# Optimization experiments

Hardware: AMD Instinct MI355X
Metric: run time of the kernel (lower is better)

Reference implementation:

```python
import jax, jax.numpy as jnp
import numpy as np

DIM, NH, WS, SS = 192, 6, 8, 4
B, H, W = 4, 192, 192
MID = max(DIM // 16, 4)
N = WS * WS
HD = DIM // NH
SCALE = HD ** -0.5

def _rel_index():
    coords = np.stack(np.meshgrid(np.arange(WS), np.arange(WS), indexing='ij')).reshape(2, -1)
    rel = (coords[:, :, None] - coords[:, None, :]).transpose(1, 2, 0)
    rel[..., 0] += WS - 1
    rel[..., 1] += WS - 1
    rel[..., 0] *= 2 * WS - 1
    return rel.sum(-1)  # (N, N)

REL_IDX = jnp.asarray(_rel_index())

def _shift_mask():
    img = np.zeros((1, H, W, 1), np.float32)
    sl = (slice(0, -WS), slice(-WS, -SS), slice(-SS, None))
    cnt = 0
    for hs in sl:
        for ws_ in sl:
            img[:, hs, ws_, :] = cnt
            cnt += 1
    mw = img.reshape(1, H // WS, WS, W // WS, WS, 1).transpose(0, 1, 3, 2, 4, 5).reshape(-1, N)
    am = mw[:, None, :] - mw[:, :, None]
    return jnp.asarray(np.where(am != 0, -100.0, 0.0).astype(np.float32))  # (nW, N, N)

MASK = _shift_mask()

def _win_part(x):  # (B,H,W,C) -> (B*nW, N, C)
    Bb, Hh, Ww, C = x.shape
    x = x.reshape(Bb, Hh // WS, WS, Ww // WS, WS, C).transpose(0, 1, 3, 2, 4, 5)
    return x.reshape(-1, N, C)

def _win_rev(x, Bb):  # (B*nW, N, C) -> (B,H,W,C)
    x = x.reshape(Bb, H // WS, W // WS, WS, WS, -1).transpose(0, 1, 3, 2, 4, 5)
    return x.reshape(Bb, H, W, -1)

def _ln(x, g, b):
    mu = x.mean(-1, keepdims=True)
    var = ((x - mu) ** 2).mean(-1, keepdims=True)
    return (x - mu) * jax.lax.rsqrt(var + 1e-5) * g + b

def _conv(x, w, b, groups=1):
    y = jax.lax.conv_general_dilated(x, w, (1, 1), 'SAME',
        dimension_numbers=('NCHW', 'OIHW', 'NCHW'), feature_group_count=groups)
    return y + b[None, :, None, None]

def _gelu(x):
    return jax.nn.gelu(x, approximate=False)  # torch default GELU is exact erf


def setup_inputs() -> dict:
    key = jax.random.key(0)
    ks = jax.random.split(key, 12)
    s = 0.02
    return {
        'x': jax.random.normal(ks[0], (B, DIM, H, W), jnp.float32),
        'norm1_g': jnp.ones((DIM,), jnp.float32),
        'norm1_b': jnp.zeros((DIM,), jnp.float32),
        'qkv_w': jax.random.normal(ks[1], (3 * DIM, DIM), jnp.float32) * s,
        'qkv_b': jnp.zeros((3 * DIM,), jnp.float32),
        'rel_table': jax.random.normal(ks[2], ((2 * WS - 1) ** 2, NH), jnp.float32) * s,
        'norm2_g': jnp.ones((DIM,), jnp.float32),
        'norm2_b': jnp.zeros((DIM,), jnp.float32),
        'mlp_w1': jax.random.normal(ks[3], (4 * DIM, DIM), jnp.float32) * s,
        'mlp_b1': jnp.zeros((4 * DIM,), jnp.float32),
        'mlp_w2': jax.random.normal(ks[4], (DIM, 4 * DIM), jnp.float32) * s,
        'mlp_b2': jnp.zeros((DIM,), jnp.float32),
        'ca_c1_w': jax.random.normal(ks[5], (DIM, DIM, 3, 3), jnp.float32) * s,
        'ca_c1_b': jnp.zeros((DIM,), jnp.float32),
        'ca_c2_w': jax.random.normal(ks[6], (DIM, DIM, 3, 3), jnp.float32) * s,
        'ca_c2_b': jnp.zeros((DIM,), jnp.float32),
        'se_w1': jax.random.normal(ks[7], (MID, DIM), jnp.float32) * s,
        'se_b1': jnp.zeros((MID,), jnp.float32),
        'se_w2': jax.random.normal(ks[8], (DIM, MID), jnp.float32) * s,
        'se_b2': jnp.zeros((DIM,), jnp.float32),
        'gate_w': jax.random.normal(ks[9], (DIM, 1, 3, 3), jnp.float32) * s,
        'gate_b': jnp.zeros((DIM,), jnp.float32),
    }


def reference(x, norm1_g, norm1_b, qkv_w, qkv_b, rel_table, norm2_g, norm2_b,
              mlp_w1, mlp_b1, mlp_w2, mlp_b2, ca_c1_w, ca_c1_b, ca_c2_w, ca_c2_b,
              se_w1, se_b1, se_w2, se_b2, gate_w, gate_b):
    Bb = x.shape[0]
    shortcut = x
    xh = _ln(x.transpose(0, 2, 3, 1), norm1_g, norm1_b)  # (B,H,W,C)
    xh = jnp.roll(xh, (-SS, -SS), (1, 2))                # shifted windows
    xw = _win_part(xh)                                   # (B*nW, N, C)
    qkv = jnp.einsum('bnc,dc->bnd', xw, qkv_w) + qkv_b
    qkv = qkv.reshape(-1, N, 3, NH, HD).transpose(2, 0, 3, 1, 4)
    q, k, v = qkv[0], qkv[1], qkv[2]                     # (B_, NH, N, HD)
    attn = jnp.einsum('bhnd,bhmd->bhnm', q * SCALE, k)
    bias = rel_table[REL_IDX.reshape(-1)].reshape(N, N, NH).transpose(2, 0, 1)
    attn = attn + bias[None]
    nW = MASK.shape[0]
    attn = attn.reshape(Bb, nW, NH, N, N) + MASK[None, :, None]
    attn = jax.nn.softmax(attn.reshape(-1, NH, N, N), axis=-1)
    out = jnp.einsum('bhnm,bhmd->bhnd', attn, v).transpose(0, 2, 1, 3).reshape(-1, N, DIM)
    # NOTE: original forward never applies self.proj; faithfully omitted.
    xh = _win_rev(out, Bb)
    xh = jnp.roll(xh, (SS, SS), (1, 2))
    x = shortcut + xh.transpose(0, 3, 1, 2)
    x = x + _conv(x, gate_w, gate_b, groups=DIM)         # depthwise conv gate
    # channel attention (conv body + SE)
    res = x
    y = _conv(x, ca_c1_w, ca_c1_b)
    y = _gelu(y)
    y = _conv(y, ca_c2_w, ca_c2_b)
    p = y.mean((2, 3))                                   # global avg pool -> (B,C)
    wgt = jax.nn.sigmoid(jax.nn.relu(p @ se_w1.T + se_b1) @ se_w2.T + se_b2)
    x = y * wgt[:, :, None, None] + res
    # MLP
    res = x
    xh = _ln(x.transpose(0, 2, 3, 1), norm2_g, norm2_b)
    xh = _gelu(jnp.einsum('bhwc,dc->bhwd', xh, mlp_w1) + mlp_b1)
    xh = jnp.einsum('bhwd,cd->bhwc', xh, mlp_w2) + mlp_b2
    return res + xh.transpose(0, 3, 1, 2)
```

## Files before the change

kernel.cpp:

```cpp
#include <hip/hip_runtime.h>
#include <hip/hip_bf16.h>

#define NWIN 576
#define SP 36864
#define ATT_SCALE 0.17677669529663687f

typedef unsigned short u16;
typedef unsigned int u32;
typedef __attribute__((ext_vector_type(8))) __bf16 bf16x8;
typedef __attribute__((ext_vector_type(4))) float f32x4;

__device__ __forceinline__ float b2f(u16 u){ return __uint_as_float(((u32)u)<<16); }
__device__ __forceinline__ u16 f2b(float f){ u32 u = __float_as_uint(f); return (u16)((u + 0x7FFFu + ((u>>16)&1u)) >> 16); }
__device__ __forceinline__ float fast_rcp(float d){ float r; asm("v_rcp_f32 %0, %1" : "=v"(r) : "v"(d)); return r; }
__device__ __forceinline__ u32 cvtpk(float lo, float hi){ u32 r; asm("v_cvt_pk_bf16_f32 %0, %1, %2" : "=v"(r) : "v"(lo), "v"(hi)); return r; }
__device__ __forceinline__ float gelu_f(float v){
  float u = v*(1.5957691216f + 0.0713548163f*v*v);
  return v * fast_rcp(1.0f + __expf(-u));
}
__device__ __forceinline__ f32x4 mfma16(bf16x8 a, bf16x8 b, f32x4 c){
  return __builtin_amdgcn_mfma_f32_16x16x32_bf16(a, b, c, 0, 0, 0);
}

__global__ __launch_bounds__(256) void k_transpose(const float* __restrict__ x, u16* __restrict__ xn){
  __shared__ float tile[32][33];
  int blk = blockIdx.x;
  int b = blk / 1728; int rem = blk % 1728;
  int hg = rem / 36; int rem2 = rem % 36;
  int wt = rem2 / 6, ct = rem2 % 6;
  int t = threadIdx.x;
  int lw = t & 31, g = t >> 5;
  for (int r4 = 0; r4 < 4; ++r4){
    int h = hg*4 + r4;
    for (int r = 0; r < 4; ++r){
      int cl = g + r*8;
      tile[cl][lw] = x[(((size_t)b*192 + ct*32 + cl)*192 + h)*192 + wt*32 + lw];
    }
    __syncthreads();
    for (int r = 0; r < 4; ++r){
      int wl = g + r*8;
      xn[(((size_t)b*192 + h)*192 + wt*32 + wl)*192 + ct*32 + lw] = f2b(tile[lw][wl]);
    }
    __syncthreads();
  }
}

__global__ __launch_bounds__(256) void k_prep_all(
    const float* __restrict__ c1w, const float* __restrict__ c2w,
    const float* __restrict__ qkv_w, const float* __restrict__ rel_table,
    const float* __restrict__ mlp_w1, const float* __restrict__ mlp_w2,
    const float* __restrict__ n2g, const float* __restrict__ n2b, const float* __restrict__ mb1,
    u16* __restrict__ Wpk1, u16* __restrict__ Wpk2, u16* __restrict__ Qkvpk,
    float* __restrict__ biasT, u16* __restrict__ W1pk, u16* __restrict__ W2pk,
    float* __restrict__ w1gd, float* __restrict__ wcv){
  int i = blockIdx.x*256 + threadIdx.x;
  if (i < 331776){
    int j = i & 7; int l = (i >> 3) & 63; int rem = i >> 9;
    int nt = rem % 12; int rem2 = rem / 12; int kc = rem2 % 6; int tap = rem2 / 6;
    int ci = kc*32 + ((l>>4)<<3) + j;
    int co = nt*16 + (l & 15);
    Wpk1[i] = f2b(c1w[(co*192 + ci)*9 + tap]);
    Wpk2[i] = f2b(c2w[(co*192 + ci)*9 + tap]);
    return;
  }
  i -= 331776;
  if (i < 110592){
    int j = i & 7; int l = (i >> 3) & 63; int rem = i >> 9;
    int kc = rem % 6; int nt = rem / 6;
    int row = nt*16 + (l & 15); int c = kc*32 + ((l>>4)<<3) + j;
    Qkvpk[i] = f2b(qkv_w[row*192 + c]);
    return;
  }
  i -= 110592;
  if (i < 24576){
    int q = i & 63; int k = (i>>6) & 63; int h = i >> 12;
    int di = (q>>3) - (k>>3) + 7; int dj = (q&7) - (k&7) + 7;
    biasT[i] = rel_table[(di*15 + dj)*6 + h];
    return;
  }
  i -= 24576;
  if (i < 147456){
    int j = i & 7; int l = (i >> 3) & 63; int rem = i >> 9;
    int kc = rem % 6; int nt = rem / 6;
    int ho = nt*16 + (l & 15); int ci = kc*32 + ((l>>4)<<3) + j;
    W1pk[i] = f2b(mlp_w1[ho*192 + ci] * n2g[ci]);
    return;
  }
  i -= 147456;
  if (i < 147456){
    int j = i & 7; int l = (i >> 3) & 63; int rem = i >> 9;
    int kc = rem % 24; int nt = rem / 24;
    int co = nt*16 + (l & 15); int ho = kc*32 + ((l>>4)<<3) + j;
    W2pk[i] = f2b(mlp_w2[co*768 + ho]);
    return;
  }
  i -= 147456;
  if (i < 768){
    float sg = 0.f, sb = 0.f;
    const float* row = mlp_w1 + (size_t)i*192;
    for (int ci = 0; ci < 192; ++ci){ float w = row[ci]; sg += w*n2g[ci]; sb += w*n2b[ci]; }
    w1gd[i] = sg; wcv[i] = sb + mb1[i];
  }
}

__global__ __launch_bounds__(768, 3) void k_attn(const float* __restrict__ x, const u16* __restrict__ xn, int use_xn,
    const float* __restrict__ g1, const float* __restrict__ be1,
    const u16* __restrict__ qkvpk, const float* __restrict__ qkv_b,
    const float* __restrict__ biasT, u16* __restrict__ x1)
{
  __shared__ u16 xw[12800];
  __shared__ u16 qs[6][64][40];
  __shared__ u16 ks[6][64][40];
  __shared__ u16 vt[6][32][72];
  __shared__ int ih[64], iw[64], rid[64];
  __shared__ float red[64][12], red2[64][12], mu[64], rsg[64];
  int blk = blockIdx.x, t = threadIdx.x;
  int b = blk / NWIN, wi = blk % NWIN, wy = wi / 24, wx = wi % 24;
  int wid = t >> 6, l = t & 63, l15 = l & 15, lg = l >> 4;
  if (t < 64){
    int i = t >> 3, j = t & 7;
    int gh = wy*8 + i, gw = wx*8 + j;
    int hf = gh + 4; if (hf >= 192) hf -= 192;
    int wf = gw + 4; if (wf >= 192) wf -= 192;
    ih[t] = hf; iw[t] = wf;
    int rh = (gh < 184) ? 0 : ((gh < 188) ? 1 : 2);
    int rw = (gw < 184) ? 0 : ((gw < 188) ? 1 : 2);
    rid[t] = rh*3 + rw;
  }
  __syncthreads();
  if (use_xn){
    for (int idx = t; idx < 1536; idx += 768){
      int n = idx / 24, q = idx % 24;
      *(uint4*)&xw[n*200 + q*8] =
        *(const uint4*)(xn + ((size_t)((b*192 + ih[n])*192 + iw[n]))*192 + q*8);
    }
  } else {
    for (int idx = t; idx < 12288; idx += 768){
      int n = idx & 63, c = idx >> 6;
      xw[n*200 + c] = f2b(x[(((size_t)b*192 + c)*192 + ih[n])*192 + iw[n]]);
    }
  }
  __syncthreads();
  { int n = t / 12, part = t % 12;
    float s = 0.f, s2 = 0.f;
    for (int c = part*16; c < part*16 + 16; ++c){ float v = b2f(xw[n*200 + c]); s += v; s2 += v*v; }
    red[n][part] = s; red2[n][part] = s2; }
  __syncthreads();
  if (t < 64){
    float s = 0.f, s2 = 0.f;
    #pragma unroll
    for (int p = 0; p < 12; ++p){ s += red[t][p]; s2 += red2[t][p]; }
    float m = s * (1.f/192.f);
    float v = s2 * (1.f/192.f) - m*m;
    mu[t] = m; rsg[t] = rsqrtf(v + 1e-5f);
  }
  __syncthreads();
  for (int idx = t; idx < 12288; idx += 768){
    int n = idx & 63, c = idx >> 6;
    float v = (b2f(xw[n*200 + c]) - mu[n]) * rsg[n] * g1[c] + be1[c];
    xw[n*200 + c] = f2b(v);
  }
  __syncthreads();
  {
    f32x4 acc[3][4];
    #pragma unroll
    for (int i3 = 0; i3 < 3; ++i3)
      #pragma unroll
      for (int mt = 0; mt < 4; ++mt) acc[i3][mt] = (f32x4){0.f,0.f,0.f,0.f};
    #pragma unroll
    for (int kc = 0; kc < 6; ++kc){
      bf16x8 a4[4];
      #pragma unroll
      for (int mt = 0; mt < 4; ++mt)
        a4[mt] = *(const bf16x8*)&xw[(mt*16 + l15)*200 + kc*32 + lg*8];
      #pragma unroll
      for (int i3 = 0; i3 < 3; ++i3){
        int ntg = wid*3 + i3;
        bf16x8 bf = *(const bf16x8*)(qkvpk + ((size_t)ntg*6 + kc)*512 + l*8);
        #pragma unroll
        for (int mt = 0; mt < 4; ++mt)
          acc[i3][mt] = mfma16(a4[mt], bf, acc[i3][mt]);
      }
    }
    #pragma unroll
    for (int i3 = 0; i3 < 3; ++i3){
      int ntg = wid*3 + i3;
      float bv = qkv_b[ntg*16 + l15];
      int m = ntg/12, hh = (ntg%12)>>1, hd0 = (ntg&1)*16;
      #pragma unroll
      for (int mt = 0; mt < 4; ++mt)
        #pragma unroll
        for (int r = 0; r < 4; ++r){
          int tok = mt*16 + lg*4 + r;
          float val = acc[i3][mt][r] + bv;
          if (m == 0){ qs[hh][tok][hd0 + l15] = f2b(val * ATT_SCALE); }
          else if (m == 1){ ks[hh][tok][hd0 + l15] = f2b(val); }
          else { vt[hh][hd0 + l15][tok] = f2b(val); }
        }
    }
  }
  __syncthreads();
  int h = wid >> 1, mt0 = (wid & 1) * 2;
  f32x4 st[2][4];
  {
    bf16x8 bq0 = *(const bf16x8*)&qs[h][(mt0  )*16 + l15][lg*8];
    bf16x8 bq1 = *(const bf16x8*)&qs[h][(mt0+1)*16 + l15][lg*8];
    #pragma unroll
    for (int nt = 0; nt < 4; ++nt){
      bf16x8 ak = *(const bf16x8*)&ks[h][nt*16 + l15][lg*8];
      st[0][nt] = mfma16(ak, bq0, (f32x4){0.f,0.f,0.f,0.f});
      st[1][nt] = mfma16(ak, bq1, (f32x4){0.f,0.f,0.f,0.f});
    }
  }
  u32 pk[2][4][2];
  #pragma unroll
  for (int m2 = 0; m2 < 2; ++m2){
    int qg = (mt0 + m2)*16 + l15;
    int rq = rid[qg];
    const float* bp = biasT + (size_t)h*4096 + qg;
    float mx = -1e30f;
    #pragma unroll
    for (int nt = 0; nt < 4; ++nt)
      #pragma unroll
      for (int r = 0; r < 4; ++r){
        int kg = nt*16 + lg*4 + r;
        float v = st[m2][nt][r] + bp[kg*64] + (rq != rid[kg] ? -100.f : 0.f);
        st[m2][nt][r] = v;
        mx = fmaxf(mx, v);
      }
    mx = fmaxf(mx, __shfl_xor(mx, 16));
    mx = fmaxf(mx, __shfl_xor(mx, 32));
    float ssum = 0.f;
    #pragma unroll
    for (int nt = 0; nt < 4; ++nt)
      #pragma unroll
      for (int r = 0; r < 4; ++r){
        float e = __expf(st[m2][nt][r] - mx);
        st[m2][nt][r] = e; ssum += e;
      }
    ssum += __shfl_xor(ssum, 16);
    ssum += __shfl_xor(ssum, 32);
    float inv = fast_rcp(ssum);
    #pragma unroll
    for (int nt = 0; nt < 4; ++nt){
      pk[m2][nt][0] = cvtpk(st[m2][nt][0]*inv, st[m2][nt][1]*inv);
      pk[m2][nt][1] = cvtpk(st[m2][nt][2]*inv, st[m2][nt][3]*inv);
    }
  }
  f32x4 o[2][2];
  #pragma unroll
  for (int m2 = 0; m2 < 2; ++m2)
    #pragma unroll
    for (int nd = 0; nd < 2; ++nd) o[m2][nd] = (f32x4){0.f,0.f,0.f,0.f};
  {
    int srcA = ((lg & 1) << 1)*16 + l15;
    bool hiSel = (lg & 2) != 0;
    #pragma unroll
    for (int kc = 0; kc < 2; ++kc){
      bf16x8 bv0 = *(const bf16x8*)&vt[h][l15][kc*32 + lg*8];
      bf16x8 bv1 = *(const bf16x8*)&vt[h][16 + l15][kc*32 + lg*8];
      #pragma unroll
      for (int m2 = 0; m2 < 2; ++m2){
        u32 q0 = __shfl((int)pk[m2][2*kc  ][0], srcA);
        u32 q1 = __shfl((int)pk[m2][2*kc+1][0], srcA);
        u32 q2 = __shfl((int)pk[m2][2*kc  ][1], srcA);
        u32 q3 = __shfl((int)pk[m2][2*kc+1][1], srcA);
        u32 q4 = __shfl((int)pk[m2][2*kc  ][0], srcA + 16);
        u32 q5 = __shfl((int)pk[m2][2*kc+1][0], srcA + 16);
        u32 q6 = __shfl((int)pk[m2][2*kc  ][1], srcA + 16);
        u32 q7 = __shfl((int)pk[m2][2*kc+1][1], srcA + 16);
        union { u32 u[4]; bf16x8 v; } ap;
        ap.u[0] = hiSel ? q1 : q0;
        ap.u[1] = hiSel ? q3 : q2;
        ap.u[2] = hiSel ? q5 : q4;
        ap.u[3] = hiSel ? q7 : q6;
        o[m2][0] = mfma16(ap.v, bv0, o[m2][0]);
        o[m2][1] = mfma16(ap.v, bv1, o[m2][1]);
      }
    }
  }
  #pragma unroll
  for (int m2 = 0; m2 < 2; ++m2)
    #pragma unroll
    for (int nd = 0; nd < 2; ++nd)
      #pragma unroll
      for (int r = 0; r < 4; ++r){
        int tok = (mt0 + m2)*16 + lg*4 + r;
        xw[tok*200 + h*32 + nd*16 + l15] = f2b(o[m2][nd][r]);
      }
  __syncthreads();
  if (use_xn){
    for (int idx = t; idx < 1536; idx += 768){
      int n = idx / 24, q = idx % 24;
      size_t tokoff = (size_t)((b*192 + ih[n])*192 + iw[n]);
      uint4 xv = *(const uint4*)(xn + tokoff*192 + q*8);
      uint4 ov = *(const uint4*)&xw[n*200 + q*8];
      uint4 res;
      u32* xp = (u32*)&xv; u32* op = (u32*)&ov; u32* rp = (u32*)&res;
      #pragma unroll
      for (int w2 = 0; w2 < 4; ++w2){
        float a0 = b2f((u16)(xp[w2] & 0xffffu)) + b2f((u16)(op[w2] & 0xffffu));
        float a1 = b2f((u16)(xp[w2] >> 16))    + b2f((u16)(op[w2] >> 16));
        rp[w2] = (u32)f2b(a0) | ((u32)f2b(a1) << 16);
      }
      *(uint4*)(x1 + tokoff*192 + q*8) = res;
    }
  } else {
    for (int idx = t; idx < 12288; idx += 768){
      int n = idx & 63, c = idx >> 6;
      size_t tokoff = (size_t)((b*192 + ih[n])*192 + iw[n]);
      float sc = x[(((size_t)b*192 + c)*192 + ih[n])*192 + iw[n]];
      x1[tokoff*192 + c] = f2b(sc + b2f(xw[n*200 + c]));
    }
  }
}

__global__ __launch_bounds__(192) void k_gate(const u16* __restrict__ x1, const float* __restrict__ gw,
                                              const float* __restrict__ gb, u16* __restrict__ x2){
  int bid = blockIdx.x;
  int blk = (bid & 7) * 2304 + (bid >> 3);
  int wt = blk % 24; int rem = blk / 24;
  int h = rem % 192; int b = rem / 192;
  int c = threadIdx.x;
  int w0 = wt*8;
  float wr[9];
  #pragma unroll
  for (int p = 0; p < 9; ++p) wr[p] = gw[c*9 + p];
  float bias = gb[c];
  float in[3][10];
  #pragma unroll
  for (int dy = 0; dy < 3; ++dy){
    int hh = h + dy - 1;
    bool hok = (hh >= 0 && hh < 192);
    #pragma unroll
    for (int p = 0; p < 10; ++p){
      int ww = w0 + p - 1;
      bool ok = hok && (ww >= 0 && ww < 192);
      in[dy][p] = ok ? b2f(x1[(((size_t)b*192 + hh)*192 + ww)*192 + c]) : 0.f;
    }
  }
  size_t rowbase = ((size_t)b*192 + h)*192;
  #pragma unroll
  for (int i = 0; i < 8; ++i){
    float acc = bias;
    #pragma unroll
    for (int dy = 0; dy < 3; ++dy)
      #pragma unroll
      for (int dx = 0; dx < 3; ++dx)
        acc += in[dy][i + dx] * wr[dy*3 + dx];
    float v = in[1][i + 1] + acc;
    x2[(rowbase + w0 + i)*192 + c] = f2b(v);
  }
}

__global__ __launch_bounds__(256) void k_conv(const u16* __restrict__ src, const u16* __restrict__ wpk,
                                              const float* __restrict__ cb, u16* __restrict__ dst,
                                              int do_gelu, float* __restrict__ pp){
  __shared__ u16 tin[20592];
  int bid = blockIdx.x;
  int blk = (bid & 7) * 288 + (bid >> 3);
  int b = blk / 576; int rem = blk % 576;
  int h = rem / 3; int w0 = (rem % 3) * 64;
  int t = threadIdx.x;
  int wid = t >> 6, l = t & 63;
  int l15 = l & 15, lg = l >> 4;
  f32x4 acc[4][3];
  #pragma unroll
  for (int mt = 0; mt < 4; ++mt)
    #pragma unroll
    for (int j = 0; j < 3; ++j) acc[mt][j] = (f32x4){0.f,0.f,0.f,0.f};
  for (int ch = 0; ch < 2; ++ch){
    __syncthreads();
    for (int idx = t; idx < 2376; idx += 256){
      int r = idx / 792; int r2 = idx % 792; int p = r2 / 12; int q = r2 % 12;
      int hh = h + r - 1, ww = w0 + p - 1;
      uint4 v = make_uint4(0u,0u,0u,0u);
      if (hh >= 0 && hh < 192 && ww >= 0 && ww < 192)
        v = *(const uint4*)(src + (((size_t)(b*192 + hh))*192 + ww)*192 + ch*96 + q*8);
      *(uint4*)&tin[(r*66 + p)*104 + q*8] = v;
    }
    __syncthreads();
    for (int dy = 0; dy < 3; ++dy){
      for (int kch = 0; kch < 3; ++kch){
        bf16x8 af[4][3];
        #pragma unroll
        for (int mt = 0; mt < 4; ++mt)
          #pragma unroll
          for (int dx = 0; dx < 3; ++dx)
            af[mt][dx] = *(const bf16x8*)&tin[(dy*66 + mt*16 + l15 + dx)*104 + kch*32 + lg*8];
        bf16x8 bw[3][3];
        int kc = ch*3 + kch;
        #pragma unroll
        for (int dx = 0; dx < 3; ++dx)
          #pragma unroll
          for (int j = 0; j < 3; ++j)
            bw[dx][j] = *(const bf16x8*)(wpk + ((((size_t)(dy*3+dx)*6 + kc)*12 + wid*3 + j)*64 + l)*8);
        __builtin_amdgcn_s_setprio(1);
        #pragma unroll
        for (int dx = 0; dx < 3; ++dx)
          #pragma unroll
          for (int j = 0; j < 3; ++j)
            #pragma unroll
            for (int mt = 0; mt < 4; ++mt)
              acc[mt][j] = mfma16(af[mt][dx], bw[dx][j], acc[mt][j]);
        __builtin_amdgcn_s_setprio(0);
      }
    }
  }
  __syncthreads();
  float bv[3];
  #pragma unroll
  for (int j = 0; j < 3; ++j) bv[j] = cb[wid*48 + j*16 + l15];
  #pragma unroll
  for (int mt = 0; mt < 4; ++mt)
    #pragma unroll
    for (int j = 0; j < 3; ++j)
      #pragma unroll
      for (int r = 0; r < 4; ++r){
        int pix = mt*16 + lg*4 + r;
        float v = acc[mt][j][r] + bv[j];
        if (do_gelu) v = gelu_f(v);
        tin[pix*200 + wid*48 + j*16 + l15] = f2b(v);
      }
  __syncthreads();
  for (int idx = t; idx < 1536; idx += 256){
    int pix = idx / 24, q = idx % 24;
    *(uint4*)(dst + (((size_t)(b*192 + h))*192 + w0 + pix)*192 + q*8) = *(const uint4*)&tin[pix*200 + q*8];
  }
  if (pp){
    if (t < 192){
      float s = 0.f;
      #pragma unroll 8
      for (int pix = 0; pix < 64; ++pix) s += b2f(tin[pix*200 + t]);
      pp[(size_t)blk*192 + t] = s;
    }
  }
}

__global__ __launch_bounds__(256) void k_se(const float* __restrict__ pp, const float* __restrict__ w1,
    const float* __restrict__ bb1, const float* __restrict__ w2, const float* __restrict__ bb2,
    float* __restrict__ wgt){
  __shared__ float pb[192]; __shared__ float hq[12];
  int t = threadIdx.x;
  int b = blockIdx.x;
  if (t < 192){
    float s = 0.f;
    const float* base = pp + (size_t)b*576*192 + t;
    for (int ch = 0; ch < 576; ++ch) s += base[ch*192];
    pb[t] = s * (1.f/36864.f);
  }
  __syncthreads();
  if (t < 12){ float a = bb1[t]; for (int c = 0; c < 192; ++c) a += pb[c]*w1[t*192 + c]; hq[t] = fmaxf(a, 0.f); }
  __syncthreads();
  if (t < 192){ float a = bb2[t]; for (int m = 0; m < 12; ++m) a += hq[m]*w2[t*12 + m]; wgt[b*192 + t] = 1.f/(1.f + __expf(-a)); }
}

__global__ __launch_bounds__(256) void k_combine(const u16* __restrict__ y2, const u16* __restrict__ x2,
                                                 const float* __restrict__ wgt, u16* __restrict__ x3){
  size_t e = ((size_t)blockIdx.x*256 + threadIdx.x)*4;
  int c = (int)(e % 192);
  int b = (int)(e / ((size_t)SP*192));
  uint2 ya = *(const uint2*)(y2 + e);
  uint2 xa = *(const uint2*)(x2 + e);
  float4 wf = *(const float4*)(wgt + b*192 + c);
  float r0 = b2f((u16)(ya.x & 0xffffu))*wf.x + b2f((u16)(xa.x & 0xffffu));
  float r1 = b2f((u16)(ya.x >> 16))   *wf.y + b2f((u16)(xa.x >> 16));
  float r2 = b2f((u16)(ya.y & 0xffffu))*wf.z + b2f((u16)(xa.y & 0xffffu));
  float r3 = b2f((u16)(ya.y >> 16))   *wf.w + b2f((u16)(xa.y >> 16));
  uint2 o; o.x = (u32)f2b(r0) | ((u32)f2b(r1)<<16); o.y = (u32)f2b(r2) | ((u32)f2b(r3)<<16);
  *(uint2*)(x3 + e) = o;
}

__global__ __launch_bounds__(256, 2) void k_mlp(const u16* __restrict__ src0, const u16* __restrict__ src1,
    const float* __restrict__ wgt, int fused, const u16* __restrict__ W1pk,
    const float* __restrict__ w1gd, const float* __restrict__ wcv,
    const u16* __restrict__ W2pk, const float* __restrict__ mb2,
    float* __restrict__ out){
  __shared__ u16 lnS[32][200];
  __shared__ u16 hidH[32*384];
  __shared__ float mu[32], rsg[32];
  int blk = blockIdx.x, t = threadIdx.x;
  int b = blk / 1152; int rem = blk % 1152;
  int h = rem / 6; int w0 = (rem % 6) * 32;
  size_t tokbase = ((size_t)b*192 + h)*192 + w0;
  int wid = t >> 6, l = t & 63, l15 = l & 15, lg = l >> 4;
  char* hb = (char*)hidH;
  if (fused){
    for (int idx = t; idx < 768; idx += 256){
      int tok = idx / 24, q = idx % 24;
      uint4 yv = *(const uint4*)(src0 + (tokbase + tok)*192 + q*8);
      uint4 xv = *(const uint4*)(src1 + (tokbase + tok)*192 + q*8);
      const float* wb = wgt + b*192 + q*8;
      uint4 res;
      u32* yp = (u32*)&yv; u32* xp = (u32*)&xv; u32* rp = (u32*)&res;
      #pragma unroll
      for (int w2 = 0; w2 < 4; ++w2){
        float r0 = b2f((u16)(yp[w2] & 0xffffu))*wb[2*w2]   + b2f((u16)(xp[w2] & 0xffffu));
        float r1 = b2f((u16)(yp[w2] >> 16))   *wb[2*w2+1] + b2f((u16)(xp[w2] >> 16));
        rp[w2] = cvtpk(r0, r1);
      }
      *(uint4*)&lnS[tok][q*8] = res;
    }
  } else {
    for (int idx = t; idx < 768; idx += 256){
      int tok = idx / 24, q = idx % 24;
      *(uint4*)&lnS[tok][q*8] = *(const uint4*)(src0 + (tokbase + tok)*192 + q*8);
    }
  }
  __syncthreads();
  { int tok = t >> 3, part = t & 7;
    float s = 0.f, s2 = 0.f;
    #pragma unroll
    for (int i = 0; i < 3; ++i){
      uint4 v = *(const uint4*)&lnS[tok][part*8 + 64*i];
      u32* vp = (u32*)&v;
      #pragma unroll
      for (int q = 0; q < 4; ++q){
        float a = b2f((u16)(vp[q] & 0xffffu)), c2 = b2f((u16)(vp[q] >> 16));
        s += a + c2; s2 += a*a + c2*c2;
      }
    }
    #pragma unroll
    for (int d = 1; d < 8; d <<= 1){
      s  += __shfl_xor(s, d);
      s2 += __shfl_xor(s2, d);
    }
    if (part == 0){
      float m = s*(1.f/192.f); float v = s2*(1.f/192.f) - m*m;
      mu[tok] = m; rsg[tok] = rsqrtf(v + 1e-5f);
    } }
  __syncthreads();
  float rsgL[2], rmuL[2];
  rsgL[0] = rsg[l15];      rmuL[0] = rsgL[0]*mu[l15];
  rsgL[1] = rsg[16 + l15]; rmuL[1] = rsgL[1]*mu[16 + l15];
  bf16x8 bT[2][6];
  #pragma unroll
  for (int tt = 0; tt < 2; ++tt)
    #pragma unroll
    for (int kc = 0; kc < 6; ++kc)
      bT[tt][kc] = *(const bf16x8*)&lnS[tt*16 + l15][kc*32 + lg*8];
  int nb = wid*3;
  f32x4 acc2[2][3];
  #pragma unroll
  for (int mt = 0; mt < 2; ++mt)
    #pragma unroll
    for (int j = 0; j < 3; ++j) acc2[mt][j] = (f32x4){0.f,0.f,0.f,0.f};
  #pragma unroll
  for (int ph = 0; ph < 2; ++ph){
    #pragma unroll
    for (int i = 0; i < 6; ++i){
      int hot = ph*24 + wid*6 + i;
      bf16x8 aw[6];
      #pragma unroll
      for (int kc = 0; kc < 6; ++kc)
        aw[kc] = *(const bf16x8*)(W1pk + ((size_t)(hot*6 + kc)*64 + l)*8);
      float4 gd = *(const float4*)(w1gd + hot*16 + lg*4);
      float4 wc4 = *(const float4*)(wcv + hot*16 + lg*4);
      int hoL = (wid*6 + i)*16 + lg*4;
      #pragma unroll
      for (int tt = 0; tt < 2; ++tt){
        f32x4 acc = (f32x4){0.f,0.f,0.f,0.f};
        __builtin_amdgcn_s_setprio(1);
        #pragma unroll
        for (int kc = 0; kc < 6; ++kc)
          acc = mfma16(aw[kc], bT[tt][kc], acc);
        __builtin_amdgcn_s_setprio(0);
        float h0 = fmaf(rsgL[tt], acc[0], fmaf(-rmuL[tt], gd.x, wc4.x));
        float h1 = fmaf(rsgL[tt], acc[1], fmaf(-rmuL[tt], gd.y, wc4.y));
        float h2 = fmaf(rsgL[tt], acc[2], fmaf(-rmuL[tt], gd.z, wc4.z));
        float h3 = fmaf(rsgL[tt], acc[3], fmaf(-rmuL[tt], gd.w, wc4.w));
        u32 p0 = cvtpk(gelu_f(h0), gelu_f(h1));
        u32 p1 = cvtpk(gelu_f(h2), gelu_f(h3));
        int tok = tt*16 + l15;
        int byt = (tok*768 + hoL*2) ^ ((l15 & 7) << 4);
        *(uint2*)(hb + byt) = make_uint2(p0, p1);
      }
    }
    __syncthreads();
    #pragma unroll 2
    for (int kc = 0; kc < 12; ++kc){
      int by0 = ((      l15)*768 + (kc*32 + lg*8)*2) ^ ((l15 & 7) << 4);
      int by1 = ((16 +  l15)*768 + (kc*32 + lg*8)*2) ^ ((l15 & 7) << 4);
      bf16x8 a0 = *(const bf16x8*)(hb + by0);
      bf16x8 a1 = *(const bf16x8*)(hb + by1);
      bf16x8 bw3[3];
      #pragma unroll
      for (int j = 0; j < 3; ++j)
        bw3[j] = *(const bf16x8*)(W2pk + (((size_t)(nb + j)*24 + ph*12 + kc)*64 + l)*8);
      __builtin_amdgcn_s_setprio(1);
      #pragma unroll
      for (int j = 0; j < 3; ++j){
        acc2[0][j] = mfma16(a0, bw3[j], acc2[0][j]);
        acc2[1][j] = mfma16(a1, bw3[j], acc2[1][j]);
      }
      __builtin_amdgcn_s_setprio(0);
    }
    __syncthreads();
  }
  #pragma unroll
  for (int j = 0; j < 3; ++j){
    int co = (nb + j)*16 + l15;
    float bj = mb2[co];
    #pragma unroll
    for (int mt = 0; mt < 2; ++mt){
      int tok0 = mt*16 + lg*4;
      float4 ov;
      #pragma unroll
      for (int r = 0; r < 4; ++r)
        ((float*)&ov)[r] = b2f(lnS[tok0 + r][co]) + acc2[mt][j][r] + bj;
      *(float4*)(out + (((size_t)b*192 + co)*192 + h)*192 + w0 + tok0) = ov;
    }
  }
}

extern "C" void kernel_launch(void* const* d_in, const int* in_sizes, int n_in,
                              void* d_out, int out_size, void* d_ws, size_t ws_size,
                              hipStream_t stream){
  const float* x      = (const float*)d_in[0];
  const float* n1g    = (const float*)d_in[1];
  const float* n1b    = (const float*)d_in[2];
  const float* qkv_w  = (const float*)d_in[3];
  const float* qkv_b  = (const float*)d_in[4];
  const float* rel_t  = (const float*)d_in[5];
  const float* n2g    = (const float*)d_in[6];
  const float* n2b    = (const float*)d_in[7];
  const float* mlp_w1 = (const float*)d_in[8];
  const float* mlp_b1 = (const float*)d_in[9];
  const float* mlp_w2 = (const float*)d_in[10];
  const float* mlp_b2 = (const float*)d_in[11];
  const float* c1w    = (const float*)d_in[12];
  const float* c1b    = (const float*)d_in[13];
  const float* c2w    = (const float*)d_in[14];
  const float* c2b    = (const float*)d_in[15];
  const float* sew1   = (const float*)d_in[16];
  const float* seb1   = (const float*)d_in[17];
  const float* sew2   = (const float*)d_in[18];
  const float* seb2   = (const float*)d_in[19];
  const float* gw     = (const float*)d_in[20];
  const float* gb     = (const float*)d_in[21];

  const size_t E  = (size_t)4*192*192*192;
  const size_t EB = E*2;
  const size_t SMALL = 663552*2 + 221184 + 98304 + 294912*2 + 4*576*192*4 + 768*4*3 + 65536;
  char* ws = (char*)d_ws;
  u16* ws0 = (u16*)(ws);
  u16* ws1 = (u16*)(ws + EB);
  size_t off = 2*EB;
  int use_xn = (ws_size >= 3*EB + SMALL) ? 1 : 0;
  u16* xn = nullptr;
  if (use_xn){ xn = (u16*)(ws + off); off += EB; }
  u16* Wpk1  = (u16*)(ws + off); off += 663552;
  u16* Wpk2  = (u16*)(ws + off); off += 663552;
  u16* Qkvpk = (u16*)(ws + off); off += 221184;
  float* biasT = (float*)(ws + off); off += 98304;
  u16* W1pk = (u16*)(ws + off); off += 294912;
  u16* W2pk = (u16*)(ws + off); off += 294912;
  float* w1gd = (float*)(ws + off); off += 768*4;
  float* wcv  = (float*)(ws + off); off += 768*4;
  float* pp  = (float*)(ws + off); off += (size_t)4*576*192*4;
  float* wgt = (float*)(ws + off); off += 768*4;

  if (use_xn) k_transpose<<<6912, 256, 0, stream>>>(x, xn);
  k_prep_all<<<2979, 256, 0, stream>>>(c1w, c2w, qkv_w, rel_t, mlp_w1, mlp_w2,
                                       n2g, n2b, mlp_b1,
                                       Wpk1, Wpk2, Qkvpk, biasT, W1pk, W2pk, w1gd, wcv);

  k_attn<<<2304, 768, 0, stream>>>(x, xn, use_xn, n1g, n1b, Qkvpk, qkv_b, biasT, ws0);
  k_gate<<<18432, 192, 0, stream>>>(ws0, gw, gb, ws1);
  k_conv<<<2304, 256, 0, stream>>>(ws1, Wpk1, c1b, ws0, 1, nullptr);
  u16* y2 = use_xn ? xn : (u16*)d_out;
  k_conv<<<2304, 256, 0, stream>>>(ws0, Wpk2, c2b, y2, 0, pp);
  k_se<<<4, 256, 0, stream>>>(pp, sew1, seb1, sew2, seb2, wgt);
  if (use_xn){
    k_mlp<<<4608, 256, 0, stream>>>(y2, ws1, wgt, 1, W1pk, w1gd, wcv, W2pk, mlp_b2, (float*)d_out);
  } else {
    k_combine<<<27648, 256, 0, stream>>>((const u16*)d_out, ws1, wgt, ws0);
    k_mlp<<<4608, 256, 0, stream>>>(ws0, ws0, wgt, 0, W1pk, w1gd, wcv, W2pk, mlp_b2, (float*)d_out);
  }
}
```

Measured before the change: 582.9 us.

## Double MLP token tile to 64 and split hidden dimension into four phases

The MLP kernel now handles 64 tokens per block instead of 32, and runs the 768-wide hidden dimension in four 192-wide phases instead of two 384-wide ones. Each W1/W2 weight fragment loaded from global memory is reused across twice as many tokens, which halves weight traffic per token. The cost is more accumulator registers (4x3 tiles) plus held weight fragments, which may lower occupancy under launch_bounds(256,2). It also adds an extra synchronisation round per block, and the grid shrinks to 2304 blocks.

```diff
diff --git a/kernel.cpp b/kernel.cpp
--- a/kernel.cpp
+++ b/kernel.cpp
@@ -476,17 +476,17 @@
     const float* __restrict__ w1gd, const float* __restrict__ wcv,
     const u16* __restrict__ W2pk, const float* __restrict__ mb2,
     float* __restrict__ out){
-  __shared__ u16 lnS[32][200];
-  __shared__ u16 hidH[32*384];
-  __shared__ float mu[32], rsg[32];
+  __shared__ u16 lnS[64][200];
+  __shared__ u16 hidQ[64*192];
+  __shared__ float mu[64], rsg[64];
   int blk = blockIdx.x, t = threadIdx.x;
-  int b = blk / 1152; int rem = blk % 1152;
-  int h = rem / 6; int w0 = (rem % 6) * 32;
+  int b = blk / 576; int rem = blk % 576;
+  int h = rem / 3; int w0 = (rem % 3) * 64;
   size_t tokbase = ((size_t)b*192 + h)*192 + w0;
   int wid = t >> 6, l = t & 63, l15 = l & 15, lg = l >> 4;
-  char* hb = (char*)hidH;
+  char* hb = (char*)hidQ;
   if (fused){
-    for (int idx = t; idx < 768; idx += 256){
+    for (int idx = t; idx < 1536; idx += 256){
       int tok = idx / 24, q = idx % 24;
       uint4 yv = *(const uint4*)(src0 + (tokbase + tok)*192 + q*8);
       uint4 xv = *(const uint4*)(src1 + (tokbase + tok)*192 + q*8);
@@ -502,17 +502,17 @@
       *(uint4*)&lnS[tok][q*8] = res;
     }
   } else {
-    for (int idx = t; idx < 768; idx += 256){
+    for (int idx = t; idx < 1536; idx += 256){
       int tok = idx / 24, q = idx % 24;
       *(uint4*)&lnS[tok][q*8] = *(const uint4*)(src0 + (tokbase + tok)*192 + q*8);
     }
   }
   __syncthreads();
-  { int tok = t >> 3, part = t & 7;
+  { int tok = t >> 2, part = t & 3;
     float s = 0.f, s2 = 0.f;
     #pragma unroll
-    for (int i = 0; i < 3; ++i){
-      uint4 v = *(const uint4*)&lnS[tok][part*8 + 64*i];
+    for (int i = 0; i < 6; ++i){
+      uint4 v = *(const uint4*)&lnS[tok][part*8 + 32*i];
       u32* vp = (u32*)&v;
       #pragma unroll
       for (int q = 0; q < 4; ++q){
@@ -521,7 +521,7 @@
       }
     }
     #pragma unroll
-    for (int d = 1; d < 8; d <<= 1){
+    for (int d = 1; d < 4; d <<= 1){
       s  += __shfl_xor(s, d);
       s2 += __shfl_xor(s2, d);
     }
@@ -530,69 +530,76 @@
       mu[tok] = m; rsg[tok] = rsqrtf(v + 1e-5f);
     } }
   __syncthreads();
-  float rsgL[2], rmuL[2];
-  rsgL[0] = rsg[l15];      rmuL[0] = rsgL[0]*mu[l15];
-  rsgL[1] = rsg[16 + l15]; rmuL[1] = rsgL[1]*mu[16 + l15];
-  bf16x8 bT[2][6];
-  #pragma unroll
-  for (int tt = 0; tt < 2; ++tt)
-    #pragma unroll
-    for (int kc = 0; kc < 6; ++kc)
-      bT[tt][kc] = *(const bf16x8*)&lnS[tt*16 + l15][kc*32 + lg*8];
+  float rsgL[4], rmuL[4];
+  #pragma unroll
+  for (int tt = 0; tt < 4; ++tt){
+    rsgL[tt] = rsg[tt*16 + l15];
+    rmuL[tt] = rsgL[tt]*mu[tt*16 + l15];
+  }
   int nb = wid*3;
-  f32x4 acc2[2][3];
-  #pragma unroll
-  for (int mt = 0; mt < 2; ++mt)
+  f32x4 acc2[4][3];
+  #pragma unroll
+  for (int mt = 0; mt < 4; ++mt)
     #pragma unroll
     for (int j = 0; j < 3; ++j) acc2[mt][j] = (f32x4){0.f,0.f,0.f,0.f};
   #pragma unroll
-  for (int ph = 0; ph < 2; ++ph){
-    #pragma unroll
-    for (int i = 0; i < 6; ++i){
-      int hot = ph*24 + wid*6 + i;
-      bf16x8 aw[6];
+  for (int ph = 0; ph < 4; ++ph){
+    bf16x8 aw[3][6];
+    float4 gd[3], wc4[3];
+    #pragma unroll
+    for (int i = 0; i < 3; ++i){
+      int hot = ph*12 + wid*3 + i;
       #pragma unroll
       for (int kc = 0; kc < 6; ++kc)
-        aw[kc] = *(const bf16x8*)(W1pk + ((size_t)(hot*6 + kc)*64 + l)*8);
-      float4 gd = *(const float4*)(w1gd + hot*16 + lg*4);
-      float4 wc4 = *(const float4*)(wcv + hot*16 + lg*4);
-      int hoL = (wid*6 + i)*16 + lg*4;
-      #pragma unroll
-      for (int tt = 0; tt < 2; ++tt){
+        aw[i][kc] = *(const bf16x8*)(W1pk + ((size_t)(hot*6 + kc)*64 + l)*8);
+      gd[i]  = *(const float4*)(w1gd + hot*16 + lg*4);
+      wc4[i] = *(const float4*)(wcv + hot*16 + lg*4);
+    }
+    #pragma unroll
+    for (int tt = 0; tt < 4; ++tt){
+      bf16x8 bT[6];
+      #pragma unroll
+      for (int kc = 0; kc < 6; ++kc)
+        bT[kc] = *(const bf16x8*)&lnS[tt*16 + l15][kc*32 + lg*8];
+      #pragma unroll
+      for (int i = 0; i < 3; ++i){
         f32x4 acc = (f32x4){0.f,0.f,0.f,0.f};
         __builtin_amdgcn_s_setprio(1);
         #pragma unroll
         for (int kc = 0; kc < 6; ++kc)
-          acc = mfma16(aw[kc], bT[tt][kc], acc);
+          acc = mfma16(aw[i][kc], bT[kc], acc);
         __builtin_amdgcn_s_setprio(0);
-        float h0 = fmaf(rsgL[tt], acc[0], fmaf(-rmuL[tt], gd.x, wc4.x));
-        float h1 = fmaf(rsgL[tt], acc[1], fmaf(-rmuL[tt], gd.y, wc4.y));
-        float h2 = fmaf(rsgL[tt], acc[2], fmaf(-rmuL[tt], gd.z, wc4.z));
-        float h3 = fmaf(rsgL[tt], acc[3], fmaf(-rmuL[tt], gd.w, wc4.w));
+        float h0 = fmaf(rsgL[tt], acc[0], fmaf(-rmuL[tt], gd[i].x, wc4[i].x));
+        float h1 = fmaf(rsgL[tt], acc[1], fmaf(-rmuL[tt], gd[i].y, wc4[i].y));
+        float h2 = fmaf(rsgL[tt], acc[2], fmaf(-rmuL[tt], gd[i].z, wc4[i].z));
+        float h3 = fmaf(rsgL[tt], acc[3], fmaf(-rmuL[tt], gd[i].w, wc4[i].w));
         u32 p0 = cvtpk(gelu_f(h0), gelu_f(h1));
         u32 p1 = cvtpk(gelu_f(h2), gelu_f(h3));
         int tok = tt*16 + l15;
-        int byt = (tok*768 + hoL*2) ^ ((l15 & 7) << 4);
+        int hoL = (wid*3 + i)*16 + lg*4;
+        int byt = (tok*384 + hoL*2) ^ ((l15 & 7) << 4);
         *(uint2*)(hb + byt) = make_uint2(p0, p1);
       }
     }
     __syncthreads();
     #pragma unroll 2
-    for (int kc = 0; kc < 12; ++kc){
-      int by0 = ((      l15)*768 + (kc*32 + lg*8)*2) ^ ((l15 & 7) << 4);
-      int by1 = ((16 +  l15)*768 + (kc*32 + lg*8)*2) ^ ((l15 & 7) << 4);
-      bf16x8 a0 = *(const bf16x8*)(hb + by0);
-      bf16x8 a1 = *(const bf16x8*)(hb + by1);
+    for (int kc = 0; kc < 6; ++kc){
+      bf16x8 a[4];
+      #pragma unroll
+      for (int mt = 0; mt < 4; ++mt){
+        int by = ((mt*16 + l15)*384 + (kc*32 + lg*8)*2) ^ ((l15 & 7) << 4);
+        a[mt] = *(const bf16x8*)(hb + by);
+      }
       bf16x8 bw3[3];
       #pragma unroll
       for (int j = 0; j < 3; ++j)
-        bw3[j] = *(const bf16x8*)(W2pk + (((size_t)(nb + j)*24 + ph*12 + kc)*64 + l)*8);
+        bw3[j] = *(const bf16x8*)(W2pk + (((size_t)(nb + j)*24 + ph*6 + kc)*64 + l)*8);
       __builtin_amdgcn_s_setprio(1);
       #pragma unroll
-      for (int j = 0; j < 3; ++j){
-        acc2[0][j] = mfma16(a0, bw3[j], acc2[0][j]);
-        acc2[1][j] = mfma16(a1, bw3[j], acc2[1][j]);
-      }
+      for (int j = 0; j < 3; ++j)
+        #pragma unroll
+        for (int mt = 0; mt < 4; ++mt)
+          acc2[mt][j] = mfma16(a[mt], bw3[j], acc2[mt][j]);
       __builtin_amdgcn_s_setprio(0);
     }
     __syncthreads();
@@ -602,7 +609,7 @@
     int co = (nb + j)*16 + l15;
     float bj = mb2[co];
     #pragma unroll
-    for (int mt = 0; mt < 2; ++mt){
+    for (int mt = 0; mt < 4; ++mt){
       int tok0 = mt*16 + lg*4;
       float4 ov;
       #pragma unroll
@@ -672,9 +679,9 @@
   k_conv<<<2304, 256, 0, stream>>>(ws0, Wpk2, c2b, y2, 0, pp);
   k_se<<<4, 256, 0, stream>>>(pp, sew1, seb1, sew2, seb2, wgt);
   if (use_xn){
-    k_mlp<<<4608, 256, 0, stream>>>(y2, ws1, wgt, 1, W1pk, w1gd, wcv, W2pk, mlp_b2, (float*)d_out);
+    k_mlp<<<2304, 256, 0, stream>>>(y2, ws1, wgt, 1, W1pk, w1gd, wcv, W2pk, mlp_b2, (float*)d_out);
   } else {
     k_combine<<<27648, 256, 0, stream>>>((const u16*)d_out, ws1, wgt, ws0);
-    k_mlp<<<4608, 256, 0, stream>>>(ws0, ws0, wgt, 0, W1pk, w1gd, wcv, W2pk, mlp_b2, (float*)d_out);
-  }
-}
+    k_mlp<<<2304, 256, 0, stream>>>(ws0, ws0, wgt, 0, W1pk, w1gd, wcv, W2pk, mlp_b2, (float*)d_out);
+  }
+}
```

Measured after the change: 579.8 us. No clear change (-0.5%).
